# Optimization experiments

Hardware: AMD Instinct MI355X
Metric: run time of the kernel (lower is better)

Reference implementation:

```python
import jax, jax.numpy as jnp
import numpy as np

N_NODES = 50000
N_EDGES = 500000
EDGE_DIM = 16
DIM = 128          # num_features == hidden == 128 so all layers share shapes
N_LAYERS = 3
N_GRAPHS = 512
N_CLASSES = 10
BN_EPS = 1e-5


def _bn(x, g, b, rm, rv):
    # eval-mode BatchNorm1d
    return (x - rm) * jax.lax.rsqrt(rv + BN_EPS) * g + b


def setup_inputs() -> dict:
    key = jax.random.key(0)
    ks = jax.random.split(key, 32)
    s = 0.05
    inp = {
        "x": jax.random.normal(ks[0], (N_NODES, DIM), jnp.float32),
        "edge_attr": jax.random.normal(ks[1], (N_EDGES, EDGE_DIM), jnp.float32),
        "edge_index": jax.random.randint(ks[2], (2, N_EDGES), 0, N_NODES, jnp.int64),
        "batch": jnp.sort(jax.random.randint(ks[3], (N_NODES,), 0, N_GRAPHS, jnp.int64)),
        # edge encoder params (stacked over layers)
        "ee_w1": jax.random.normal(ks[4], (N_LAYERS, EDGE_DIM, DIM), jnp.float32) * s,
        "ee_b1": jax.random.normal(ks[5], (N_LAYERS, DIM), jnp.float32) * s,
        "ee_w2": jax.random.normal(ks[6], (N_LAYERS, DIM, DIM), jnp.float32) * s,
        "ee_b2": jax.random.normal(ks[7], (N_LAYERS, DIM), jnp.float32) * s,
        "ee_bn_g": 1.0 + 0.1 * jax.random.normal(ks[8], (N_LAYERS, DIM), jnp.float32),
        "ee_bn_b": 0.1 * jax.random.normal(ks[9], (N_LAYERS, DIM), jnp.float32),
        "ee_bn_rm": 0.1 * jax.random.normal(ks[10], (N_LAYERS, DIM), jnp.float32),
        "ee_bn_rv": jax.random.uniform(ks[11], (N_LAYERS, DIM), jnp.float32, 0.5, 1.5),
        # node MLP params (stacked over layers)
        "mlp_w1": jax.random.normal(ks[12], (N_LAYERS, DIM, DIM), jnp.float32) * s,
        "mlp_b1": jax.random.normal(ks[13], (N_LAYERS, DIM), jnp.float32) * s,
        "mlp_w2": jax.random.normal(ks[14], (N_LAYERS, DIM, DIM), jnp.float32) * s,
        "mlp_b2": jax.random.normal(ks[15], (N_LAYERS, DIM), jnp.float32) * s,
        "mlp_bn_g": 1.0 + 0.1 * jax.random.normal(ks[16], (N_LAYERS, DIM), jnp.float32),
        "mlp_bn_b": 0.1 * jax.random.normal(ks[17], (N_LAYERS, DIM), jnp.float32),
        "mlp_bn_rm": 0.1 * jax.random.normal(ks[18], (N_LAYERS, DIM), jnp.float32),
        "mlp_bn_rv": jax.random.uniform(ks[19], (N_LAYERS, DIM), jnp.float32, 0.5, 1.5),
        # readout heads
        "lin1_w": jax.random.normal(ks[20], (DIM, DIM), jnp.float32) * s,
        "lin1_b": jax.random.normal(ks[21], (DIM,), jnp.float32) * s,
        "lin2_w": jax.random.normal(ks[22], (DIM, N_CLASSES), jnp.float32) * s,
        "lin2_b": jax.random.normal(ks[23], (N_CLASSES,), jnp.float32) * s,
    }
    return inp


def _forward(x, edge_attr, ee_w1, ee_b1, ee_w2, ee_b2, ee_bn_g, ee_bn_b, ee_bn_rm, ee_bn_rv,
             mlp_w1, mlp_b1, mlp_w2, mlp_b2, mlp_bn_g, mlp_bn_b, mlp_bn_rm, mlp_bn_rv,
             lin1_w, lin1_b, lin2_w, lin2_b, edge_index, batch):
    src, dst = edge_index[0], edge_index[1]  # x_j gathered from src, aggregated at dst
    n_nodes = x.shape[0]
    for i in range(N_LAYERS):
        # edge encoder: Linear -> ReLU -> Linear -> ReLU -> BN
        e = jax.nn.relu(edge_attr @ ee_w1[i] + ee_b1[i])
        e = jax.nn.relu(e @ ee_w2[i] + ee_b2[i])
        e = _bn(e, ee_bn_g[i], ee_bn_b[i], ee_bn_rm[i], ee_bn_rv[i])
        # message: relu(x_j + edge_emb), aggregate: scatter-add to dst
        msg = jax.nn.relu(x[src] + e)                         # [E, DIM]
        agg = jax.ops.segment_sum(msg, dst, num_segments=n_nodes)
        # mlp(x + agg): Linear -> ReLU -> Linear -> ReLU -> BN
        h = x + agg
        h = jax.nn.relu(h @ mlp_w1[i] + mlp_b1[i])
        h = jax.nn.relu(h @ mlp_w2[i] + mlp_b2[i])
        x = _bn(h, mlp_bn_g[i], mlp_bn_b[i], mlp_bn_rm[i], mlp_bn_rv[i])
    # global mean pool over graphs
    sums = jax.ops.segment_sum(x, batch, num_segments=N_GRAPHS)          # [G, DIM]
    cnts = jax.ops.segment_sum(jnp.ones((n_nodes, 1), x.dtype), batch, num_segments=N_GRAPHS)
    pooled = sums / jnp.maximum(cnts, 1.0)
    h = jax.nn.relu(pooled @ lin1_w + lin1_b)   # dropout off in eval mode
    logits = h @ lin2_w + lin2_b
    return jax.nn.log_softmax(logits, axis=-1)


def reference(x, edge_attr, ee_w1, ee_b1, ee_w2, ee_b2, ee_bn_g, ee_bn_b, ee_bn_rm, ee_bn_rv,
              mlp_w1, mlp_b1, mlp_w2, mlp_b2, mlp_bn_g, mlp_bn_b, mlp_bn_rm, mlp_bn_rv,
              lin1_w, lin1_b, lin2_w, lin2_b, edge_index, batch):
    return _forward(x, edge_attr, ee_w1, ee_b1, ee_w2, ee_b2, ee_bn_g, ee_bn_b, ee_bn_rm, ee_bn_rv,
                    mlp_w1, mlp_b1, mlp_w2, mlp_b2, mlp_bn_g, mlp_bn_b, mlp_bn_rm, mlp_bn_rv,
                    lin1_w, lin1_b, lin2_w, lin2_b, edge_index, batch)
```

## Files before the change

### kernel.cpp

```cpp
#include <hip/hip_runtime.h>

#define N_NODES_C 50000
#define N_EDGES_C 500000
#define EDGE_DIM_C 16
#define DIM_C 128
#define N_LAYERS_C 3
#define N_GRAPHS_C 512
#define N_CLASSES_C 10
#define BN_EPS_C 1e-5f

#define SCAN_NB ((N_NODES_C + 1023) / 1024)

typedef short bf16x8 __attribute__((ext_vector_type(8)));
typedef float f32x4  __attribute__((ext_vector_type(4)));

__device__ inline unsigned cvt_pk_bf16(float a, float b) {
    unsigned r;
    asm("v_cvt_pk_bf16_f32 %0, %1, %2" : "=v"(r) : "v"(a), "v"(b));
    return r;
}
__device__ inline float bf2f(unsigned short h) {
    union { unsigned u; float f; } v; v.u = ((unsigned)h) << 16;
    return v.f;
}
__device__ inline ushort4 nt_load_e4(const unsigned short* p) {
    const unsigned* q = (const unsigned*)p;
    unsigned a = __builtin_nontemporal_load(q);
    unsigned b = __builtin_nontemporal_load(q + 1);
    ushort4 r;
    r.x = (unsigned short)(a & 0xffff); r.y = (unsigned short)(a >> 16);
    r.z = (unsigned short)(b & 0xffff); r.w = (unsigned short)(b >> 16);
    return r;
}

__global__ void hist_kernel(const int* __restrict__ dst, int* __restrict__ cnt)
{
    int e = blockIdx.x * blockDim.x + threadIdx.x;
    if (e < N_EDGES_C) atomicAdd(&cnt[dst[e]], 1);
}

__global__ __launch_bounds__(1024)
void scan1_kernel(const int* __restrict__ cnt, int* __restrict__ incl,
                  int* __restrict__ bsum)
{
    __shared__ int buf[1024];
    int i = blockIdx.x * 1024 + threadIdx.x;
    int v = (i < N_NODES_C) ? cnt[i] : 0;
    buf[threadIdx.x] = v;
    __syncthreads();
    for (int off = 1; off < 1024; off <<= 1) {
        int t = (threadIdx.x >= off) ? buf[threadIdx.x - off] : 0;
        __syncthreads();
        buf[threadIdx.x] += t;
        __syncthreads();
    }
    if (i < N_NODES_C) incl[i] = buf[threadIdx.x];
    if (threadIdx.x == 1023) bsum[blockIdx.x] = buf[1023];
}

__global__ void scan2_kernel(int* __restrict__ bsum)
{
    if (threadIdx.x == 0 && blockIdx.x == 0) {
        int run = 0;
        for (int b = 0; b < SCAN_NB; ++b) { int v = bsum[b]; bsum[b] = run; run += v; }
    }
}

__global__ __launch_bounds__(1024)
void scan3_kernel(const int* __restrict__ cnt, const int* __restrict__ incl,
                  const int* __restrict__ bsum,
                  int* __restrict__ offsets, int* __restrict__ cursor)
{
    int i = blockIdx.x * 1024 + threadIdx.x;
    if (i < N_NODES_C) {
        int inc = incl[i] + bsum[blockIdx.x];
        offsets[i + 1] = inc;
        cursor[i] = inc - cnt[i];
        if (i == 0) offsets[0] = 0;
    }
}

__global__ void scatter_kernel(const int* __restrict__ src,
                               const int* __restrict__ dst,
                               const float* __restrict__ ea,
                               int* __restrict__ cursor,
                               int* __restrict__ srcPerm,
                               unsigned short* __restrict__ eaPermH)
{
    int e = blockIdx.x * blockDim.x + threadIdx.x;
    if (e >= N_EDGES_C) return;
    int pos = atomicAdd(&cursor[dst[e]], 1);
    srcPerm[pos] = src[e];
    const float4* in = (const float4*)&ea[(size_t)e * EDGE_DIM_C];
    float4 a = in[0], b = in[1], c = in[2], d = in[3];
    uint4 lo, hi;
    lo.x = cvt_pk_bf16(a.x, a.y); lo.y = cvt_pk_bf16(a.z, a.w);
    lo.z = cvt_pk_bf16(b.x, b.y); lo.w = cvt_pk_bf16(b.z, b.w);
    hi.x = cvt_pk_bf16(c.x, c.y); hi.y = cvt_pk_bf16(c.z, c.w);
    hi.z = cvt_pk_bf16(d.x, d.y); hi.w = cvt_pk_bf16(d.z, d.w);
    uint4* outp = (uint4*)&eaPermH[(size_t)pos * EDGE_DIM_C];
    outp[0] = lo; outp[1] = hi;
}

__global__ __launch_bounds__(512)
void goff_kernel(const int* __restrict__ batch, int* __restrict__ goff)
{
    int g = threadIdx.x;
    int lo = 0, hi = N_NODES_C;
    while (lo < hi) {
        int mid = (lo + hi) >> 1;
        if (batch[mid] < g) lo = mid + 1; else hi = mid;
    }
    goff[g] = lo;
    if (g == 0) goff[N_GRAPHS_C] = N_NODES_C;
}

__global__ __launch_bounds__(256)
void wprep_kernel(const float* __restrict__ ee_w1, const float* __restrict__ ee_w2,
                  const float* __restrict__ mlp_w1, const float* __restrict__ mlp_w2,
                  short* __restrict__ W1T, short* __restrict__ W2T,
                  short* __restrict__ MT1, short* __restrict__ MT2)
{
    int b = blockIdx.x;
    int l = b % 3;
    int which = b / 3;
    if (which == 0) {
        const float* in = ee_w1 + l * 16 * 128;
        short* outp = W1T + l * 128 * 16;
        for (int i = threadIdx.x; i < 2048; i += 256) {
            int f = i >> 4, k = i & 15;
            outp[i] = (short)(cvt_pk_bf16(in[k * 128 + f], 0.f) & 0xffff);
        }
    } else {
        const float* in = (which == 1 ? ee_w2 : which == 2 ? mlp_w1 : mlp_w2) + l * 128 * 128;
        short* outp = (which == 1 ? W2T : which == 2 ? MT1 : MT2) + l * 128 * 128;
        for (int i = threadIdx.x; i < 16384; i += 256) {
            int f = i >> 7, k = i & 127;
            outp[i] = (short)(cvt_pk_bf16(in[k * 128 + f], 0.f) & 0xffff);
        }
    }
}

__global__ __launch_bounds__(256)
void emb_mfma(const unsigned short* __restrict__ eaPermH,
              const short* __restrict__ W1T, const float* __restrict__ b1,
              const short* __restrict__ W2T, const float* __restrict__ b2,
              const float* __restrict__ bng, const float* __restrict__ bnb,
              const float* __restrict__ bnrm, const float* __restrict__ bnrv,
              unsigned short* __restrict__ emb, int c0, int chunkN)
{
    __shared__ short t1s[64 * 128];

    const int tid  = threadIdx.x;
    const int lane = tid & 63;
    const int w    = tid >> 6;
    const int ln15 = lane & 15;
    const int g    = lane >> 4;
    const int colbase = w * 32;

    bf16x8 fw1[2], fw2[2][4];
    float b1v[2], b2v[2], scv[2], shv[2];
    #pragma unroll
    for (int ct = 0; ct < 2; ++ct) {
        int f = colbase + ct * 16 + ln15;
        if (g < 2) fw1[ct] = *(const bf16x8*)&W1T[f * 16 + g * 8];
        else       fw1[ct] = (bf16x8){0,0,0,0,0,0,0,0};
        #pragma unroll
        for (int kb = 0; kb < 4; ++kb)
            fw2[ct][kb] = *(const bf16x8*)&W2T[f * 128 + kb * 32 + g * 8];
        b1v[ct] = b1[f]; b2v[ct] = b2[f];
        float sc = bng[f] * rsqrtf(bnrv[f] + BN_EPS_C);
        scv[ct] = sc; shv[ct] = bnb[f] - bnrm[f] * sc;
    }

    const int niter = (chunkN + 63) / 64;
    for (int it = blockIdx.x; it < niter; it += gridDim.x) {
        const int eb = it * 64;

        #pragma unroll
        for (int rt = 0; rt < 4; ++rt) {
            bf16x8 af;
            if (g < 2) {
                int erow = min(eb + rt * 16 + ln15, chunkN - 1);
                af = *(const bf16x8*)&eaPermH[(size_t)(c0 + erow) * EDGE_DIM_C + g * 8];
            } else {
                af = (bf16x8){0,0,0,0,0,0,0,0};
            }
            #pragma unroll
            for (int ct = 0; ct < 2; ++ct) {
                f32x4 a1 = { b1v[ct], b1v[ct], b1v[ct], b1v[ct] };
                a1 = __builtin_amdgcn_mfma_f32_16x16x32_bf16(af, fw1[ct], a1, 0, 0, 0);
                int col = colbase + ct * 16 + ln15;
                #pragma unroll
                for (int r = 0; r < 4; ++r) {
                    int row = rt * 16 + g * 4 + r;
                    int idx = (row * 128 + col) ^ ((row & 15) << 3);
                    t1s[idx] = (short)(cvt_pk_bf16(fmaxf(a1[r], 0.f), 0.f) & 0xffff);
                }
            }
        }
        __syncthreads();

        f32x4 acc[4][2];
        #pragma unroll
        for (int rt = 0; rt < 4; ++rt)
            #pragma unroll
            for (int ct = 0; ct < 2; ++ct)
                acc[rt][ct] = (f32x4){ b2v[ct], b2v[ct], b2v[ct], b2v[ct] };

        #pragma unroll
        for (int rt = 0; rt < 4; ++rt) {
            bf16x8 a[4];
            int row = rt * 16 + ln15;
            #pragma unroll
            for (int kb = 0; kb < 4; ++kb) {
                int idx = (row * 128 + kb * 32 + g * 8) ^ ((row & 15) << 3);
                a[kb] = *(const bf16x8*)&t1s[idx];
            }
            #pragma unroll
            for (int ct = 0; ct < 2; ++ct)
                #pragma unroll
                for (int kb = 0; kb < 4; ++kb)
                    acc[rt][ct] = __builtin_amdgcn_mfma_f32_16x16x32_bf16(
                        a[kb], fw2[ct][kb], acc[rt][ct], 0, 0, 0);
        }
        __syncthreads();

        #pragma unroll
        for (int rt = 0; rt < 4; ++rt)
            #pragma unroll
            for (int ct = 0; ct < 2; ++ct) {
                int col = colbase + ct * 16 + ln15;
                #pragma unroll
                for (int r = 0; r < 4; ++r) {
                    int row = rt * 16 + g * 4 + r;
                    float v = fmaxf(acc[rt][ct][r], 0.f) * scv[ct] + shv[ct];
                    int idx = (row * 128 + col) ^ ((row & 15) << 3);
                    t1s[idx] = (short)(cvt_pk_bf16(v, 0.f) & 0xffff);
                }
            }
        __syncthreads();

        for (int i = tid; i < 1024; i += 256) {
            int row = i >> 4;
            int c8  = (i & 15) * 8;
            if (eb + row < chunkN) {
                int idx = (row * 128 + c8) ^ ((row & 15) << 3);
                bf16x8 v = *(const bf16x8*)&t1s[idx];
                *(bf16x8*)&emb[(size_t)(eb + row) * 128 + c8] = v;
            }
        }
        __syncthreads();
    }
}

__global__ __launch_bounds__(256)
void agg_kernel(const unsigned short* __restrict__ emb,
                const float* __restrict__ x,
                const int* __restrict__ srcPerm,
                const int* __restrict__ offsets,
                float* __restrict__ agg,
                int c0, int c1, int first)
{
    const int slot = threadIdx.x >> 5;
    const int l    = threadIdx.x & 31;
    const int n = blockIdx.x * 8 + slot;
    if (n >= N_NODES_C) return;

    int lo = offsets[n], hi = offsets[n + 1];
    lo = max(lo, c0); hi = min(hi, c1);

    float4 s = make_float4(0.f, 0.f, 0.f, 0.f);
    const bool any = lo < hi;
    for (int pos = lo; pos < hi; ++pos) {
        int srcn = srcPerm[pos];
        ushort4 eb = nt_load_e4(&emb[(size_t)(pos - c0) * DIM_C + l * 4]);
        float4 xv = *(const float4*)&x[(size_t)srcn * DIM_C + l * 4];
        s.x += fmaxf(xv.x + bf2f(eb.x), 0.f);
        s.y += fmaxf(xv.y + bf2f(eb.y), 0.f);
        s.z += fmaxf(xv.z + bf2f(eb.z), 0.f);
        s.w += fmaxf(xv.w + bf2f(eb.w), 0.f);
    }

    float4* ap = (float4*)&agg[(size_t)n * DIM_C + l * 4];
    if (first) {
        *ap = s;
    } else if (any) {
        float4 o = *ap;
        o.x += s.x; o.y += s.y; o.z += s.z; o.w += s.w;
        *ap = o;
    }
}

__global__ __launch_bounds__(256)
void node_fused(const float* __restrict__ in0, const float* __restrict__ in1,
                const short* __restrict__ WT1, const float* __restrict__ b1,
                const short* __restrict__ WT2, const float* __restrict__ b2,
                const float* __restrict__ bng, const float* __restrict__ bnb,
                const float* __restrict__ bnrm, const float* __restrict__ bnrv,
                float* __restrict__ out, int nrows)
{
    __shared__ short smem[2 * 64 * 128];
    short* hs  = smem;
    short* t1s = smem + 64 * 128;
    float* fout = (float*)smem;

    const int tid  = threadIdx.x;
    const int lane = tid & 63;
    const int w    = tid >> 6;
    const int ln15 = lane & 15;
    const int g    = lane >> 4;
    const int colbase = w * 32;

    bf16x8 fw1[2][4], fw2[2][4];
    float b1v[2], b2v[2], scv[2], shv[2];
    #pragma unroll
    for (int ct = 0; ct < 2; ++ct) {
        int f = colbase + ct * 16 + ln15;
        #pragma unroll
        for (int kb = 0; kb < 4; ++kb) {
            fw1[ct][kb] = *(const bf16x8*)&WT1[f * 128 + kb * 32 + g * 8];
            fw2[ct][kb] = *(const bf16x8*)&WT2[f * 128 + kb * 32 + g * 8];
        }
        b1v[ct] = b1[f]; b2v[ct] = b2[f];
        float sc = bng[f] * rsqrtf(bnrv[f] + BN_EPS_C);
        scv[ct] = sc; shv[ct] = bnb[f] - bnrm[f] * sc;
    }

    const int ntiles = (nrows + 63) / 64;
    for (int t = blockIdx.x; t < ntiles; t += gridDim.x) {
        const int base = t * 64;

        for (int i = tid; i < 2048; i += 256) {
            int row = i >> 5;
            int c4  = (i & 31) * 4;
            int rr  = min(base + row, nrows - 1);
            float4 v = *(const float4*)&in0[(size_t)rr * DIM_C + c4];
            float4 a1 = *(const float4*)&in1[(size_t)rr * DIM_C + c4];
            v.x += a1.x; v.y += a1.y; v.z += a1.z; v.w += a1.w;
            int idx = (row * 128 + c4) ^ ((row & 15) << 3);
            *(unsigned*)&hs[idx]     = cvt_pk_bf16(v.x, v.y);
            *(unsigned*)&hs[idx + 2] = cvt_pk_bf16(v.z, v.w);
        }
        __syncthreads();

        #pragma unroll
        for (int rt = 0; rt < 4; ++rt) {
            bf16x8 a[4];
            int row = rt * 16 + ln15;
            #pragma unroll
            for (int kb = 0; kb < 4; ++kb) {
                int idx = (row * 128 + kb * 32 + g * 8) ^ ((row & 15) << 3);
                a[kb] = *(const bf16x8*)&hs[idx];
            }
            #pragma unroll
            for (int ct = 0; ct < 2; ++ct) {
                f32x4 a1 = { b1v[ct], b1v[ct], b1v[ct], b1v[ct] };
                #pragma unroll
                for (int kb = 0; kb < 4; ++kb)
                    a1 = __builtin_amdgcn_mfma_f32_16x16x32_bf16(a[kb], fw1[ct][kb], a1, 0, 0, 0);
                int col = colbase + ct * 16 + ln15;
                #pragma unroll
                for (int r = 0; r < 4; ++r) {
                    int orow = rt * 16 + g * 4 + r;
                    int idx = (orow * 128 + col) ^ ((orow & 15) << 3);
                    t1s[idx] = (short)(cvt_pk_bf16(fmaxf(a1[r], 0.f), 0.f) & 0xffff);
                }
            }
        }
        __syncthreads();

        f32x4 acc[4][2];
        #pragma unroll
        for (int rt = 0; rt < 4; ++rt)
            #pragma unroll
            for (int ct = 0; ct < 2; ++ct)
                acc[rt][ct] = (f32x4){ b2v[ct], b2v[ct], b2v[ct], b2v[ct] };

        #pragma unroll
        for (int rt = 0; rt < 4; ++rt) {
            bf16x8 a[4];
            int row = rt * 16 + ln15;
            #pragma unroll
            for (int kb = 0; kb < 4; ++kb) {
                int idx = (row * 128 + kb * 32 + g * 8) ^ ((row & 15) << 3);
                a[kb] = *(const bf16x8*)&t1s[idx];
            }
            #pragma unroll
            for (int ct = 0; ct < 2; ++ct)
                #pragma unroll
                for (int kb = 0; kb < 4; ++kb)
                    acc[rt][ct] = __builtin_amdgcn_mfma_f32_16x16x32_bf16(
                        a[kb], fw2[ct][kb], acc[rt][ct], 0, 0, 0);
        }
        __syncthreads();

        #pragma unroll
        for (int rt = 0; rt < 4; ++rt)
            #pragma unroll
            for (int ct = 0; ct < 2; ++ct) {
                int col = colbase + ct * 16 + ln15;
                #pragma unroll
                for (int r = 0; r < 4; ++r) {
                    int row = rt * 16 + g * 4 + r;
                    float v = fmaxf(acc[rt][ct][r], 0.f) * scv[ct] + shv[ct];
                    fout[(row * 128 + col) ^ ((row & 15) << 2)] = v;
                }
            }
        __syncthreads();

        for (int i = tid; i < 2048; i += 256) {
            int row = i >> 5;
            int c4  = (i & 31) * 4;
            int orow = base + row;
            if (orow < nrows) {
                int idx = (row * 128 + c4) ^ ((row & 15) << 2);
                float4 v = *(const float4*)&fout[idx];
                *(float4*)&out[(size_t)orow * DIM_C + c4] = v;
            }
        }
        __syncthreads();
    }
}

__global__ __launch_bounds__(128)
void pool2_kernel(const float* __restrict__ x,
                  const int* __restrict__ goff,
                  float* __restrict__ pooled)
{
    const int g = blockIdx.x;
    const int tid = threadIdx.x;
    int lo = goff[g], hi = goff[g + 1];
    float s = 0.f;
    for (int n = lo; n < hi; ++n)
        s += x[(size_t)n * DIM_C + tid];
    float c = (float)max(hi - lo, 1);
    pooled[g * DIM_C + tid] = s / c;
}

__global__ __launch_bounds__(128)
void head_kernel(const float* __restrict__ pooled,
                 const float* __restrict__ l1w,
                 const float* __restrict__ l1b,
                 const float* __restrict__ l2w,
                 const float* __restrict__ l2b,
                 float* __restrict__ out)
{
    const int g = blockIdx.x;
    const int tid = threadIdx.x;
    __shared__ float ps[DIM_C];
    __shared__ float hsx[DIM_C];
    __shared__ float lg[N_CLASSES_C];
    __shared__ float lse;

    ps[tid] = pooled[g * DIM_C + tid];
    __syncthreads();

    float a = l1b[tid];
    for (int k = 0; k < DIM_C; ++k)
        a += ps[k] * l1w[k * DIM_C + tid];
    hsx[tid] = fmaxf(a, 0.f);
    __syncthreads();

    if (tid < N_CLASSES_C) {
        float s = l2b[tid];
        for (int f = 0; f < DIM_C; ++f)
            s += hsx[f] * l2w[f * N_CLASSES_C + tid];
        lg[tid] = s;
    }
    __syncthreads();

    if (tid == 0) {
        float m = lg[0];
        for (int cc = 1; cc < N_CLASSES_C; ++cc) m = fmaxf(m, lg[cc]);
        float s = 0.f;
        for (int cc = 0; cc < N_CLASSES_C; ++cc) s += expf(lg[cc] - m);
        lse = m + logf(s);
    }
    __syncthreads();

    if (tid < N_CLASSES_C)
        out[g * N_CLASSES_C + tid] = lg[tid] - lse;
}

extern "C" void kernel_launch(void* const* d_in, const int* in_sizes, int n_in,
                              void* d_out, int out_size, void* d_ws, size_t ws_size,
                              hipStream_t stream)
{
    const float* x         = (const float*)d_in[0];
    const float* edge_attr = (const float*)d_in[1];
    const int*   ei        = (const int*)d_in[2];
    const int*   batch     = (const int*)d_in[3];
    const float* ee_w1     = (const float*)d_in[4];
    const float* ee_b1     = (const float*)d_in[5];
    const float* ee_w2     = (const float*)d_in[6];
    const float* ee_b2     = (const float*)d_in[7];
    const float* ee_bn_g   = (const float*)d_in[8];
    const float* ee_bn_b   = (const float*)d_in[9];
    const float* ee_bn_rm  = (const float*)d_in[10];
    const float* ee_bn_rv  = (const float*)d_in[11];
    const float* mlp_w1    = (const float*)d_in[12];
    const float* mlp_b1    = (const float*)d_in[13];
    const float* mlp_w2    = (const float*)d_in[14];
    const float* mlp_b2    = (const float*)d_in[15];
    const float* mlp_bn_g  = (const float*)d_in[16];
    const float* mlp_bn_b  = (const float*)d_in[17];
    const float* mlp_bn_rm = (const float*)d_in[18];
    const float* mlp_bn_rv = (const float*)d_in[19];
    const float* lin1_w    = (const float*)d_in[20];
    const float* lin1_b    = (const float*)d_in[21];
    const float* lin2_w    = (const float*)d_in[22];
    const float* lin2_b    = (const float*)d_in[23];
    float* out = (float*)d_out;

    const int* src = ei;
    const int* dst = ei + N_EDGES_C;

    char* wsp = (char*)d_ws;
    float* x_cur = (float*)wsp;          wsp += (size_t)N_NODES_C * DIM_C * 4;
    float* agg   = (float*)wsp;          wsp += (size_t)N_NODES_C * DIM_C * 4;
    unsigned short* eaPermH = (unsigned short*)wsp;
                                         wsp += (size_t)N_EDGES_C * EDGE_DIM_C * 2;
    int* srcPerm = (int*)wsp;            wsp += (size_t)N_EDGES_C * 4;
    int* cnt     = (int*)wsp;            wsp += 200704;
    int* offsets = (int*)wsp;            wsp += 200704;
    int* cursor  = (int*)wsp;            wsp += 200704;
    int* incl    = (int*)wsp;            wsp += 200704;
    int* bsum    = (int*)wsp;            wsp += 4096;
    int* goff    = (int*)wsp;            wsp += 4096;
    float* pooled = (float*)wsp;         wsp += (size_t)N_GRAPHS_C * DIM_C * 4;
    short* W1T   = (short*)wsp;          wsp += (size_t)N_LAYERS_C * 128 * 16 * 2;
    short* W2T   = (short*)wsp;          wsp += (size_t)N_LAYERS_C * 128 * 128 * 2;
    short* MT1   = (short*)wsp;          wsp += (size_t)N_LAYERS_C * 128 * 128 * 2;
    short* MT2   = (short*)wsp;          wsp += (size_t)N_LAYERS_C * 128 * 128 * 2;
    unsigned short* emb = (unsigned short*)wsp;

    size_t used = (size_t)(wsp - (char*)d_ws);
    size_t embRows = (ws_size > used) ? (ws_size - used) / ((size_t)DIM_C * 2) : 0;
    int chunk = (int)((embRows < (size_t)N_EDGES_C) ? embRows : (size_t)N_EDGES_C);
    if (chunk < 128) chunk = 128;

    wprep_kernel<<<12, 256, 0, stream>>>(ee_w1, ee_w2, mlp_w1, mlp_w2,
                                         W1T, W2T, MT1, MT2);
    hipMemsetAsync(cnt, 0, N_NODES_C * sizeof(int), stream);
    hist_kernel<<<(N_EDGES_C + 255) / 256, 256, 0, stream>>>(dst, cnt);
    scan1_kernel<<<SCAN_NB, 1024, 0, stream>>>(cnt, incl, bsum);
    scan2_kernel<<<1, 64, 0, stream>>>(bsum);
    scan3_kernel<<<SCAN_NB, 1024, 0, stream>>>(cnt, incl, bsum, offsets, cursor);
    scatter_kernel<<<(N_EDGES_C + 255) / 256, 256, 0, stream>>>(
        src, dst, edge_attr, cursor, srcPerm, eaPermH);
    goff_kernel<<<1, 512, 0, stream>>>(batch, goff);

    const float* xin = x;
    for (int i = 0; i < N_LAYERS_C; ++i) {
        for (int c0 = 0; c0 < N_EDGES_C; c0 += chunk) {
            int c1 = min(c0 + chunk, N_EDGES_C);
            emb_mfma<<<1024, 256, 0, stream>>>(
                eaPermH,
                W1T + (size_t)i * 128 * 16, ee_b1 + i * DIM_C,
                W2T + (size_t)i * 128 * 128, ee_b2 + i * DIM_C,
                ee_bn_g + i * DIM_C, ee_bn_b + i * DIM_C,
                ee_bn_rm + i * DIM_C, ee_bn_rv + i * DIM_C,
                emb, c0, c1 - c0);
            agg_kernel<<<(N_NODES_C + 7) / 8, 256, 0, stream>>>(
                emb, xin, srcPerm, offsets, agg, c0, c1, c0 == 0 ? 1 : 0);
        }
        node_fused<<<782, 256, 0, stream>>>(
            xin, agg,
            MT1 + (size_t)i * 128 * 128, mlp_b1 + i * DIM_C,
            MT2 + (size_t)i * 128 * 128, mlp_b2 + i * DIM_C,
            mlp_bn_g + i * DIM_C, mlp_bn_b + i * DIM_C,
            mlp_bn_rm + i * DIM_C, mlp_bn_rv + i * DIM_C,
            x_cur, N_NODES_C);
        xin = x_cur;
    }

    pool2_kernel<<<N_GRAPHS_C, 128, 0, stream>>>(xin, goff, pooled);
    head_kernel<<<N_GRAPHS_C, 128, 0, stream>>>(pooled, lin1_w, lin1_b,
                                                lin2_w, lin2_b, out);
}
```

Baseline: 538.1 us.

## Split edge scatter into index scatter plus coalesced gather; emit bf16 node input from aggregation

The edge scatter now writes only (src, edge id) pairs into a permuted buffer. A separate gather kernel then reads edge attributes in destination order and writes srcPerm and the bf16 attributes with coalesced stores, replacing the old scattered 32-byte writes. When all edges fit in one chunk, the aggregation kernel adds x itself and stores the sum as bf16, so node_fused reads half the bytes and skips the second fp32 input. This adds one kernel launch and a pairPerm pass. The bf16 buffer reuses the agg storage.

New measurement: 551.8 us. +2.6%, slower.

```diff
diff --git a/kernel.cpp b/kernel.cpp
--- a/kernel.cpp
+++ b/kernel.cpp
@@ -80,18 +80,28 @@
     }
 }
 
-__global__ void scatter_kernel(const int* __restrict__ src,
-                               const int* __restrict__ dst,
-                               const float* __restrict__ ea,
-                               int* __restrict__ cursor,
-                               int* __restrict__ srcPerm,
-                               unsigned short* __restrict__ eaPermH)
+__global__ void scatter_idx_kernel(const int* __restrict__ src,
+                                   const int* __restrict__ dst,
+                                   int* __restrict__ cursor,
+                                   int2* __restrict__ pairPerm)
 {
     int e = blockIdx.x * blockDim.x + threadIdx.x;
     if (e >= N_EDGES_C) return;
     int pos = atomicAdd(&cursor[dst[e]], 1);
-    srcPerm[pos] = src[e];
-    const float4* in = (const float4*)&ea[(size_t)e * EDGE_DIM_C];
+    pairPerm[pos] = make_int2(src[e], e);
+}
+
+__global__ __launch_bounds__(256)
+void gather_ea_kernel(const int2* __restrict__ pairPerm,
+                      const float* __restrict__ ea,
+                      int* __restrict__ srcPerm,
+                      unsigned short* __restrict__ eaPermH)
+{
+    int pos = blockIdx.x * blockDim.x + threadIdx.x;
+    if (pos >= N_EDGES_C) return;
+    int2 pr = pairPerm[pos];
+    srcPerm[pos] = pr.x;
+    const float4* in = (const float4*)&ea[(size_t)pr.y * EDGE_DIM_C];
     float4 a = in[0], b = in[1], c = in[2], d = in[3];
     uint4 lo, hi;
     lo.x = cvt_pk_bf16(a.x, a.y); lo.y = cvt_pk_bf16(a.z, a.w);
@@ -260,7 +270,8 @@
                 const int* __restrict__ srcPerm,
                 const int* __restrict__ offsets,
                 float* __restrict__ agg,
-                int c0, int c1, int first)
+                unsigned short* __restrict__ hsG,
+                int c0, int c1, int first, int mode)
 {
     const int slot = threadIdx.x >> 5;
     const int l    = threadIdx.x & 31;
@@ -282,18 +293,28 @@
         s.w += fmaxf(xv.w + bf2f(eb.w), 0.f);
     }
 
-    float4* ap = (float4*)&agg[(size_t)n * DIM_C + l * 4];
-    if (first) {
-        *ap = s;
-    } else if (any) {
-        float4 o = *ap;
-        o.x += s.x; o.y += s.y; o.z += s.z; o.w += s.w;
-        *ap = o;
+    if (mode == 1) {
+        float4 xn = *(const float4*)&x[(size_t)n * DIM_C + l * 4];
+        s.x += xn.x; s.y += xn.y; s.z += xn.z; s.w += xn.w;
+        uint2 o;
+        o.x = cvt_pk_bf16(s.x, s.y);
+        o.y = cvt_pk_bf16(s.z, s.w);
+        *(uint2*)&hsG[(size_t)n * DIM_C + l * 4] = o;
+    } else {
+        float4* ap = (float4*)&agg[(size_t)n * DIM_C + l * 4];
+        if (first) {
+            *ap = s;
+        } else if (any) {
+            float4 o = *ap;
+            o.x += s.x; o.y += s.y; o.z += s.z; o.w += s.w;
+            *ap = o;
+        }
     }
 }
 
 __global__ __launch_bounds__(256)
 void node_fused(const float* __restrict__ in0, const float* __restrict__ in1,
+                const unsigned short* __restrict__ hsG,
                 const short* __restrict__ WT1, const float* __restrict__ b1,
                 const short* __restrict__ WT2, const float* __restrict__ b2,
                 const float* __restrict__ bng, const float* __restrict__ bnb,
@@ -331,16 +352,28 @@
     for (int t = blockIdx.x; t < ntiles; t += gridDim.x) {
         const int base = t * 64;
 
-        for (int i = tid; i < 2048; i += 256) {
-            int row = i >> 5;
-            int c4  = (i & 31) * 4;
-            int rr  = min(base + row, nrows - 1);
-            float4 v = *(const float4*)&in0[(size_t)rr * DIM_C + c4];
-            float4 a1 = *(const float4*)&in1[(size_t)rr * DIM_C + c4];
-            v.x += a1.x; v.y += a1.y; v.z += a1.z; v.w += a1.w;
-            int idx = (row * 128 + c4) ^ ((row & 15) << 3);
-            *(unsigned*)&hs[idx]     = cvt_pk_bf16(v.x, v.y);
-            *(unsigned*)&hs[idx + 2] = cvt_pk_bf16(v.z, v.w);
+        if (hsG) {
+            for (int i = tid; i < 2048; i += 256) {
+                int row = i >> 5;
+                int c4  = (i & 31) * 4;
+                int rr  = min(base + row, nrows - 1);
+                uint2 v = *(const uint2*)&hsG[(size_t)rr * DIM_C + c4];
+                int idx = (row * 128 + c4) ^ ((row & 15) << 3);
+                *(unsigned*)&hs[idx]     = v.x;
+                *(unsigned*)&hs[idx + 2] = v.y;
+            }
+        } else {
+            for (int i = tid; i < 2048; i += 256) {
+                int row = i >> 5;
+                int c4  = (i & 31) * 4;
+                int rr  = min(base + row, nrows - 1);
+                float4 v = *(const float4*)&in0[(size_t)rr * DIM_C + c4];
+                float4 a1 = *(const float4*)&in1[(size_t)rr * DIM_C + c4];
+                v.x += a1.x; v.y += a1.y; v.z += a1.z; v.w += a1.w;
+                int idx = (row * 128 + c4) ^ ((row & 15) << 3);
+                *(unsigned*)&hs[idx]     = cvt_pk_bf16(v.x, v.y);
+                *(unsigned*)&hs[idx + 2] = cvt_pk_bf16(v.z, v.w);
+            }
         }
         __syncthreads();
 
@@ -519,6 +552,7 @@
     char* wsp = (char*)d_ws;
     float* x_cur = (float*)wsp;          wsp += (size_t)N_NODES_C * DIM_C * 4;
     float* agg   = (float*)wsp;          wsp += (size_t)N_NODES_C * DIM_C * 4;
+    unsigned short* hsG = (unsigned short*)agg;
     unsigned short* eaPermH = (unsigned short*)wsp;
                                          wsp += (size_t)N_EDGES_C * EDGE_DIM_C * 2;
     int* srcPerm = (int*)wsp;            wsp += (size_t)N_EDGES_C * 4;
@@ -534,11 +568,13 @@
     short* MT1   = (short*)wsp;          wsp += (size_t)N_LAYERS_C * 128 * 128 * 2;
     short* MT2   = (short*)wsp;          wsp += (size_t)N_LAYERS_C * 128 * 128 * 2;
     unsigned short* emb = (unsigned short*)wsp;
+    int2* pairPerm = (int2*)emb;
 
     size_t used = (size_t)(wsp - (char*)d_ws);
     size_t embRows = (ws_size > used) ? (ws_size - used) / ((size_t)DIM_C * 2) : 0;
     int chunk = (int)((embRows < (size_t)N_EDGES_C) ? embRows : (size_t)N_EDGES_C);
     if (chunk < 128) chunk = 128;
+    const bool fullChunk = (chunk >= N_EDGES_C);
 
     wprep_kernel<<<12, 256, 0, stream>>>(ee_w1, ee_w2, mlp_w1, mlp_w2,
                                          W1T, W2T, MT1, MT2);
@@ -547,8 +583,10 @@
     scan1_kernel<<<SCAN_NB, 1024, 0, stream>>>(cnt, incl, bsum);
     scan2_kernel<<<1, 64, 0, stream>>>(bsum);
     scan3_kernel<<<SCAN_NB, 1024, 0, stream>>>(cnt, incl, bsum, offsets, cursor);
-    scatter_kernel<<<(N_EDGES_C + 255) / 256, 256, 0, stream>>>(
-        src, dst, edge_attr, cursor, srcPerm, eaPermH);
+    scatter_idx_kernel<<<(N_EDGES_C + 255) / 256, 256, 0, stream>>>(
+        src, dst, cursor, pairPerm);
+    gather_ea_kernel<<<(N_EDGES_C + 255) / 256, 256, 0, stream>>>(
+        pairPerm, edge_attr, srcPerm, eaPermH);
     goff_kernel<<<1, 512, 0, stream>>>(batch, goff);
 
     const float* xin = x;
@@ -563,15 +601,26 @@
                 ee_bn_rm + i * DIM_C, ee_bn_rv + i * DIM_C,
                 emb, c0, c1 - c0);
             agg_kernel<<<(N_NODES_C + 7) / 8, 256, 0, stream>>>(
-                emb, xin, srcPerm, offsets, agg, c0, c1, c0 == 0 ? 1 : 0);
-        }
-        node_fused<<<782, 256, 0, stream>>>(
-            xin, agg,
-            MT1 + (size_t)i * 128 * 128, mlp_b1 + i * DIM_C,
-            MT2 + (size_t)i * 128 * 128, mlp_b2 + i * DIM_C,
-            mlp_bn_g + i * DIM_C, mlp_bn_b + i * DIM_C,
-            mlp_bn_rm + i * DIM_C, mlp_bn_rv + i * DIM_C,
-            x_cur, N_NODES_C);
+                emb, xin, srcPerm, offsets, agg, hsG, c0, c1,
+                c0 == 0 ? 1 : 0, fullChunk ? 1 : 0);
+        }
+        if (fullChunk) {
+            node_fused<<<782, 256, 0, stream>>>(
+                nullptr, nullptr, hsG,
+                MT1 + (size_t)i * 128 * 128, mlp_b1 + i * DIM_C,
+                MT2 + (size_t)i * 128 * 128, mlp_b2 + i * DIM_C,
+                mlp_bn_g + i * DIM_C, mlp_bn_b + i * DIM_C,
+                mlp_bn_rm + i * DIM_C, mlp_bn_rv + i * DIM_C,
+                x_cur, N_NODES_C);
+        } else {
+            node_fused<<<782, 256, 0, stream>>>(
+                xin, agg, nullptr,
+                MT1 + (size_t)i * 128 * 128, mlp_b1 + i * DIM_C,
+                MT2 + (size_t)i * 128 * 128, mlp_b2 + i * DIM_C,
+                mlp_bn_g + i * DIM_C, mlp_bn_b + i * DIM_C,
+                mlp_bn_rm + i * DIM_C, mlp_bn_rv + i * DIM_C,
+                x_cur, N_NODES_C);
+        }
         xin = x_cur;
     }
 
```
